# Kernel optimization log

Hardware: AMD Instinct MI355X
Metric: run time of the kernel (lower is better)

Reference implementation:

```python
import jax, jax.numpy as jnp
import numpy as np

N_EMBD = 1024
N_HEAD = 16
B, T = 4, 2048

def setup_inputs() -> dict:
    key = jax.random.key(0)
    ks = jax.random.split(key, 5)
    s_attn = 1.0 / np.sqrt(N_EMBD)
    s_proj = 1.0 / np.sqrt(N_EMBD)
    return {
        "x": jax.random.normal(ks[0], (B, T, N_EMBD), dtype=jnp.float32),
        "w_attn": jax.random.uniform(ks[1], (N_EMBD, 3 * N_EMBD), jnp.float32, -s_attn, s_attn),
        "b_attn": jax.random.uniform(ks[2], (3 * N_EMBD,), jnp.float32, -s_attn, s_attn),
        "w_proj": jax.random.uniform(ks[3], (N_EMBD, N_EMBD), jnp.float32, -s_proj, s_proj),
        "b_proj": jax.random.uniform(ks[4], (N_EMBD,), jnp.float32, -s_proj, s_proj),
    }

def reference(x, w_attn, b_attn, w_proj, b_proj):
    Bx, Tx, C = x.shape
    hd = C // N_HEAD  # head dim
    qkv = x @ w_attn + b_attn                       # [B,T,3C]
    q, k, v = jnp.split(qkv, 3, axis=-1)
    # [B,T,C] -> [B,H,T,hd]
    def heads(t):
        return t.reshape(Bx, Tx, N_HEAD, hd).transpose(0, 2, 1, 3)
    q, k, v = heads(q), heads(k), heads(v)
    att = jnp.einsum('bhqd,bhkd->bhqk', q, k) * (1.0 / np.sqrt(hd))
    causal = jnp.tril(jnp.ones((Tx, Tx), dtype=bool))
    att = jnp.where(causal, att, -jnp.inf)
    att = jax.nn.softmax(att, axis=-1)
    y = jnp.einsum('bhqk,bhkd->bhqd', att, v)       # [B,H,T,hd]
    y = y.transpose(0, 2, 1, 3).reshape(Bx, Tx, C)
    return y @ w_proj + b_proj
```

## Files before the change

### kernel.cpp

```cpp
#include <hip/hip_runtime.h>
#include <cstdint>

typedef unsigned short u16;
typedef short s16x8 __attribute__((ext_vector_type(8)));
typedef short s16x4 __attribute__((ext_vector_type(4)));
typedef float f32x4 __attribute__((ext_vector_type(4)));
typedef float f32x16 __attribute__((ext_vector_type(16)));

#define B_   4
#define T_   2048
#define C_   1024
#define H_   16
#define HD_  64
#define M_   8192
#define N3_  3072

#define QSCALE 0.18033688011112042f

__device__ inline u16 f2b(float f) {
  union { float f; uint32_t u; } v; v.f = f;
  uint32_t u = v.u;
  return (u16)((u + 0x7FFFu + ((u >> 16) & 1u)) >> 16);
}

__device__ inline uint32_t cvtpk(float lo, float hi) {
  uint32_t r;
  asm("v_cvt_pk_bf16_f32 %0, %1, %2" : "=v"(r) : "v"(lo), "v"(hi));
  return r;
}

__device__ inline void gload_lds16(const void* g, void* l) {
  __builtin_amdgcn_global_load_lds(
      (const __attribute__((address_space(1))) void*)g,
      (__attribute__((address_space(3))) void*)l, 16, 0, 0);
}

__global__ __launch_bounds__(256) void cvt_f32_bf16(
    const float* __restrict__ in, u16* __restrict__ out, int n) {
  int i = (blockIdx.x * 256 + threadIdx.x) * 8;
  if (i >= n) return;
  float4 a = *(const float4*)(in + i);
  float4 b = *(const float4*)(in + i + 4);
  s16x8 r;
  r[0] = (short)f2b(a.x); r[1] = (short)f2b(a.y);
  r[2] = (short)f2b(a.z); r[3] = (short)f2b(a.w);
  r[4] = (short)f2b(b.x); r[5] = (short)f2b(b.y);
  r[6] = (short)f2b(b.z); r[7] = (short)f2b(b.w);
  *(s16x8*)(out + i) = r;
}

__global__ __launch_bounds__(256) void cvt_transpose(
    const float* __restrict__ W, u16* __restrict__ WT, int K, int N) {
  __shared__ u16 tile[64][65];
  int n0 = blockIdx.x * 64, k0 = blockIdx.y * 64;
  int j = threadIdx.x & 63, i0 = threadIdx.x >> 6;
#pragma unroll
  for (int i = i0; i < 64; i += 4)
    tile[i][j] = f2b(W[(size_t)(k0 + i) * N + n0 + j]);
  __syncthreads();
#pragma unroll
  for (int i = i0; i < 64; i += 4)
    WT[(size_t)(n0 + i) * K + k0 + j] = tile[j][i];
}

template <int MODE>
__global__ __launch_bounds__(256, 4) void gemm_bt(
    const u16* __restrict__ A, const u16* __restrict__ Bt,
    const float* __restrict__ bias, float* __restrict__ outf,
    u16* __restrict__ qo, u16* __restrict__ ko, u16* __restrict__ vo,
    int M, int N, int K) {
  __shared__ u16 As[128 * 64];
  __shared__ u16 Bs[128 * 64];

  int nwg = gridDim.x;
  int bid0 = blockIdx.x;
  int bid = (bid0 & 7) * (nwg >> 3) + (bid0 >> 3);
  int nbn = N >> 7;
  int bm = bid / nbn, bn = bid % nbn;
  int m0 = bm * 128, n0 = bn * 128;
  int tid = threadIdx.x;
  int lane = tid & 63, w = tid >> 6;
  int wm = (w >> 1) * 64, wn = (w & 1) * 64;
  int l15 = lane & 15, g = lane >> 4;

  f32x4 acc[4][4] = {};

  for (int kb = 0; kb < K; kb += 64) {
    __syncthreads();
#pragma unroll
    for (int p = 0; p < 4; ++p) {
      int idx = p * 256 + tid;
      int row = idx >> 3, pc = idx & 7;
      int sc = (pc ^ (row & 7)) * 8;
      gload_lds16(A  + (size_t)(m0 + row) * K + kb + sc, &As[idx * 8]);
      gload_lds16(Bt + (size_t)(n0 + row) * K + kb + sc, &Bs[idx * 8]);
    }
    __syncthreads();

#pragma unroll
    for (int ks = 0; ks < 2; ++ks) {
      int ck = ((g + 4 * ks) ^ (l15 & 7)) * 8;
      s16x8 af[4], bf[4];
#pragma unroll
      for (int mi = 0; mi < 4; ++mi)
        af[mi] = *(const s16x8*)&As[(wm + mi * 16 + l15) * 64 + ck];
#pragma unroll
      for (int ni = 0; ni < 4; ++ni)
        bf[ni] = *(const s16x8*)&Bs[(wn + ni * 16 + l15) * 64 + ck];
#pragma unroll
      for (int mi = 0; mi < 4; ++mi)
#pragma unroll
        for (int ni = 0; ni < 4; ++ni)
          acc[mi][ni] = __builtin_amdgcn_mfma_f32_16x16x32_bf16(
              af[mi], bf[ni], acc[mi][ni], 0, 0, 0);
    }
  }

#pragma unroll
  for (int mi = 0; mi < 4; ++mi)
#pragma unroll
    for (int ni = 0; ni < 4; ++ni) {
      int col = n0 + wn + ni * 16 + l15;
      float bv = bias[col];
      int row0 = m0 + wm + mi * 16 + g * 4;
      if (MODE == 0) {
#pragma unroll
        for (int r = 0; r < 4; ++r)
          outf[(size_t)(row0 + r) * N + col] = acc[mi][ni][r] + bv;
      } else {
        int which = col >> 10, hc = col & 1023;
        int h = hc >> 6, d = hc & 63;
        int b = row0 >> 11, t0 = row0 & 2047;
        if (which == 2) {
          s16x4 pv;
#pragma unroll
          for (int r = 0; r < 4; ++r) pv[r] = (short)f2b(acc[mi][ni][r] + bv);
          *(s16x4*)(vo + ((size_t)((b * 16 + h) * 64 + d)) * 2048 + t0) = pv;
        } else {
          u16* dst = (which == 0) ? qo : ko;
          float sc2 = (which == 0) ? QSCALE : 1.0f;
#pragma unroll
          for (int r = 0; r < 4; ++r)
            dst[(((size_t)(b * 16 + h)) * 2048 + (t0 + r)) * 64 + d] =
                f2b((acc[mi][ni][r] + bv) * sc2);
        }
      }
    }
}

__global__ __launch_bounds__(256, 3) void attn_fwd(
    const u16* __restrict__ Q, const u16* __restrict__ Kg,
    const u16* __restrict__ Vt, u16* __restrict__ Y) {
  __shared__ u16 Ks[64 * 64];
  __shared__ u16 Vs[64 * 64];

  int bid = blockIdx.x;
  int bh = bid & 63;
  int qb = 15 - (bid >> 6);
  int tid = threadIdx.x, lane = tid & 63, w = tid >> 6;
  int l31 = lane & 31, half = lane >> 5;

  const u16* Qh = Q  + (size_t)bh * T_ * HD_;
  const u16* Kh = Kg + (size_t)bh * T_ * HD_;
  const u16* Vh = Vt + (size_t)bh * HD_ * T_;

  int q0 = qb * 128;
  int qw = q0 + w * 32;
  int qrow = qw + l31;

  s16x8 qa[4];
#pragma unroll
  for (int kst = 0; kst < 4; ++kst)
    qa[kst] = *(const s16x8*)(Qh + (size_t)qrow * HD_ + kst * 16 + half * 8);

  f32x16 oacc[2] = {};
  float m = -3.0e30f, l = 0.f;

  int sr = tid >> 3, sc = tid & 7;
  int wswz = (sr & 7) << 4;
  int rswz = (l31 & 7) << 4;
  char* KsB = (char*)Ks;
  char* VsB = (char*)Vs;

  s16x8 kr0 = *(const s16x8*)(Kh + (size_t)sr * HD_ + sc * 8);
  s16x8 kr1 = *(const s16x8*)(Kh + (size_t)(sr + 32) * HD_ + sc * 8);
  s16x8 vr0 = *(const s16x8*)(Vh + (size_t)sr * T_ + sc * 8);
  s16x8 vr1 = *(const s16x8*)(Vh + (size_t)(sr + 32) * T_ + sc * 8);

  int ntile = 2 * qb + 2;
  for (int kt = 0; kt < ntile; ++kt) {
    int kvb = kt * 64;
    __syncthreads();
    *(s16x8*)(KsB + sr * 128 + ((sc * 16) ^ wswz))        = kr0;
    *(s16x8*)(KsB + (sr + 32) * 128 + ((sc * 16) ^ wswz)) = kr1;
    *(s16x8*)(VsB + sr * 128 + ((sc * 16) ^ wswz))        = vr0;
    *(s16x8*)(VsB + (sr + 32) * 128 + ((sc * 16) ^ wswz)) = vr1;
    __syncthreads();

    {
      int kvn = (kt + 1 < ntile) ? (kt + 1) * 64 : 0;
      kr0 = *(const s16x8*)(Kh + (size_t)(kvn + sr) * HD_ + sc * 8);
      kr1 = *(const s16x8*)(Kh + (size_t)(kvn + sr + 32) * HD_ + sc * 8);
      vr0 = *(const s16x8*)(Vh + (size_t)sr * T_ + kvn + sc * 8);
      vr1 = *(const s16x8*)(Vh + (size_t)(sr + 32) * T_ + kvn + sc * 8);
    }

    if (kvb > qw + 31) continue;

    f32x16 s0 = {}, s1 = {};
    __builtin_amdgcn_s_setprio(1);
#pragma unroll
    for (int kst = 0; kst < 4; ++kst) {
      s16x8 kb0 = *(const s16x8*)(KsB +
          (((l31) * 128 + kst * 32 + half * 16) ^ rswz));
      s0 = __builtin_amdgcn_mfma_f32_32x32x16_bf16(kb0, qa[kst], s0, 0, 0, 0);
      s16x8 kb1 = *(const s16x8*)(KsB +
          (((32 + l31) * 128 + kst * 32 + half * 16) ^ rswz));
      s1 = __builtin_amdgcn_mfma_f32_32x32x16_bf16(kb1, qa[kst], s1, 0, 0, 0);
    }
    __builtin_amdgcn_s_setprio(0);

    if (kvb + 63 > qw) {
#pragma unroll
      for (int r = 0; r < 16; ++r) {
        int kv0 = kvb + (r & 3) + 8 * (r >> 2) + 4 * half;
        if (kv0 > qrow) s0[r] = -1e30f;
        if (kv0 + 32 > qrow) s1[r] = -1e30f;
      }
    }

    float a0 = fmaxf(fmaxf(s0[0], s0[1]), fmaxf(s0[2], s0[3]));
    float a1 = fmaxf(fmaxf(s0[4], s0[5]), fmaxf(s0[6], s0[7]));
    float a2 = fmaxf(fmaxf(s0[8], s0[9]), fmaxf(s0[10], s0[11]));
    float a3 = fmaxf(fmaxf(s0[12], s0[13]), fmaxf(s0[14], s0[15]));
    float a4 = fmaxf(fmaxf(s1[0], s1[1]), fmaxf(s1[2], s1[3]));
    float a5 = fmaxf(fmaxf(s1[4], s1[5]), fmaxf(s1[6], s1[7]));
    float a6 = fmaxf(fmaxf(s1[8], s1[9]), fmaxf(s1[10], s1[11]));
    float a7 = fmaxf(fmaxf(s1[12], s1[13]), fmaxf(s1[14], s1[15]));
    float mx = fmaxf(fmaxf(fmaxf(a0, a1), fmaxf(a2, a3)),
                     fmaxf(fmaxf(a4, a5), fmaxf(a6, a7)));
    mx = fmaxf(mx, __shfl_xor(mx, 32, 64));

    if (!__all(mx <= m + 8.0f)) {
      float mn = fmaxf(m, mx);
      float alpha = __builtin_amdgcn_exp2f(m - mn);
      m = mn;
      l *= alpha;
#pragma unroll
      for (int i = 0; i < 16; ++i) { oacc[0][i] *= alpha; oacc[1][i] *= alpha; }
    }

    float rs = 0.f;
#pragma unroll
    for (int r = 0; r < 16; ++r) {
      float p0 = __builtin_amdgcn_exp2f(s0[r] - m);
      float p1 = __builtin_amdgcn_exp2f(s1[r] - m);
      s0[r] = p0; s1[r] = p1;
      rs += p0 + p1;
    }
    rs += __shfl_xor(rs, 32, 64);
    l += rs;

    s16x8 pb[4];
#pragma unroll
    for (int ks4 = 0; ks4 < 4; ++ks4) {
      const f32x16& sv = (ks4 < 2) ? s0 : s1;
      const int R = (ks4 & 1) * 8;
      uint32_t A0 = cvtpk(sv[R + 0], sv[R + 1]);
      uint32_t A1 = cvtpk(sv[R + 2], sv[R + 3]);
      uint32_t B0 = cvtpk(sv[R + 4], sv[R + 5]);
      uint32_t B1 = cvtpk(sv[R + 6], sv[R + 7]);
      uint32_t r0 = (uint32_t)__shfl_xor((int)(half ? A0 : B0), 32, 64);
      uint32_t r1 = (uint32_t)__shfl_xor((int)(half ? A1 : B1), 32, 64);
      union { uint32_t u[4]; s16x8 v; } pk_;
      pk_.u[0] = half ? r0 : A0;
      pk_.u[1] = half ? r1 : A1;
      pk_.u[2] = half ? B0 : r0;
      pk_.u[3] = half ? B1 : r1;
      pb[ks4] = pk_.v;
    }

    __builtin_amdgcn_s_setprio(1);
#pragma unroll
    for (int hb = 0; hb < 2; ++hb)
#pragma unroll
      for (int ks4 = 0; ks4 < 4; ++ks4) {
        s16x8 va = *(const s16x8*)(VsB +
            (((hb * 32 + l31) * 128 + ks4 * 32 + half * 16) ^ rswz));
        oacc[hb] = __builtin_amdgcn_mfma_f32_32x32x16_bf16(va, pb[ks4],
                                                           oacc[hb], 0, 0, 0);
      }
    __builtin_amdgcn_s_setprio(0);
  }

  int b = bh >> 4, h = bh & 15;
  float inv = 1.0f / l;
  u16* yrow = Y + ((size_t)b * T_ + qrow) * C_ + h * 64;
#pragma unroll
  for (int hb = 0; hb < 2; ++hb)
#pragma unroll
    for (int rg = 0; rg < 4; ++rg) {
      union { uint32_t u[2]; s16x4 v; } o;
      o.u[0] = cvtpk(oacc[hb][rg * 4 + 0] * inv, oacc[hb][rg * 4 + 1] * inv);
      o.u[1] = cvtpk(oacc[hb][rg * 4 + 2] * inv, oacc[hb][rg * 4 + 3] * inv);
      *(s16x4*)(yrow + hb * 32 + rg * 8 + half * 4) = o.v;
    }
}

extern "C" void kernel_launch(void* const* d_in, const int* in_sizes, int n_in,
                              void* d_out, int out_size, void* d_ws, size_t ws_size,
                              hipStream_t stream) {
  const float* x      = (const float*)d_in[0];
  const float* w_attn = (const float*)d_in[1];
  const float* b_attn = (const float*)d_in[2];
  const float* w_proj = (const float*)d_in[3];
  const float* b_proj = (const float*)d_in[4];
  float* out = (float*)d_out;

  u16* ws  = (u16*)d_ws;
  u16* xb  = ws;
  u16* wat = xb  + (size_t)M_ * C_;
  u16* wpt = wat + (size_t)N3_ * C_;
  u16* q   = wpt + (size_t)C_ * C_;
  u16* k   = q   + (size_t)M_ * C_;
  u16* v   = k   + (size_t)M_ * C_;
  u16* ya  = xb;

  cvt_f32_bf16<<<dim3((M_ * C_) / (256 * 8)), dim3(256), 0, stream>>>(x, xb, M_ * C_);
  cvt_transpose<<<dim3(N3_ / 64, C_ / 64), dim3(256), 0, stream>>>(w_attn, wat, C_, N3_);
  cvt_transpose<<<dim3(C_ / 64, C_ / 64), dim3(256), 0, stream>>>(w_proj, wpt, C_, C_);

  gemm_bt<1><<<dim3((M_ / 128) * (N3_ / 128)), dim3(256), 0, stream>>>(
      xb, wat, b_attn, nullptr, q, k, v, M_, N3_, C_);

  attn_fwd<<<dim3(64 * 16), dim3(256), 0, stream>>>(q, k, v, ya);

  gemm_bt<0><<<dim3((M_ / 128) * (C_ / 128)), dim3(256), 0, stream>>>(
      ya, wpt, b_proj, out, nullptr, nullptr, nullptr, M_, C_, C_);
}
```

Measured before the change: 166.5 us.

## Double-buffer attention K/V tiles in LDS with direct global-to-LDS loads

```diff
diff --git a/kernel.cpp b/kernel.cpp
--- a/kernel.cpp
+++ b/kernel.cpp
@@ -151,8 +151,8 @@
 __global__ __launch_bounds__(256, 3) void attn_fwd(
     const u16* __restrict__ Q, const u16* __restrict__ Kg,
     const u16* __restrict__ Vt, u16* __restrict__ Y) {
-  __shared__ u16 Ks[64 * 64];
-  __shared__ u16 Vs[64 * 64];
+  __shared__ u16 Ks[2][64 * 64];
+  __shared__ u16 Vs[2][64 * 64];
 
   int bid = blockIdx.x;
   int bh = bid & 63;
@@ -176,122 +176,120 @@
   f32x16 oacc[2] = {};
   float m = -3.0e30f, l = 0.f;
 
-  int sr = tid >> 3, sc = tid & 7;
-  int wswz = (sr & 7) << 4;
+  int srow = tid >> 3;
+  int sc = ((tid & 7) ^ (srow & 7)) * 8;
   int rswz = (l31 & 7) << 4;
-  char* KsB = (char*)Ks;
-  char* VsB = (char*)Vs;
-
-  s16x8 kr0 = *(const s16x8*)(Kh + (size_t)sr * HD_ + sc * 8);
-  s16x8 kr1 = *(const s16x8*)(Kh + (size_t)(sr + 32) * HD_ + sc * 8);
-  s16x8 vr0 = *(const s16x8*)(Vh + (size_t)sr * T_ + sc * 8);
-  s16x8 vr1 = *(const s16x8*)(Vh + (size_t)(sr + 32) * T_ + sc * 8);
+
+#define STAGE(bb, kvb_) do { \
+  gload_lds16(Kh + (size_t)((kvb_) + srow) * HD_ + sc,      &Ks[bb][tid * 8]); \
+  gload_lds16(Kh + (size_t)((kvb_) + 32 + srow) * HD_ + sc, &Ks[bb][(256 + tid) * 8]); \
+  gload_lds16(Vh + (size_t)srow * T_ + (kvb_) + sc,         &Vs[bb][tid * 8]); \
+  gload_lds16(Vh + (size_t)(32 + srow) * T_ + (kvb_) + sc,  &Vs[bb][(256 + tid) * 8]); \
+} while (0)
 
   int ntile = 2 * qb + 2;
+  STAGE(0, 0);
+  __syncthreads();
+
   for (int kt = 0; kt < ntile; ++kt) {
+    int cur = kt & 1;
     int kvb = kt * 64;
+    int kvn = (kt + 1 < ntile) ? (kt + 1) * 64 : 0;
+    STAGE(cur ^ 1, kvn);
+
+    if (kvb <= qw + 31) {
+      char* KsB = (char*)Ks[cur];
+      char* VsB = (char*)Vs[cur];
+
+      f32x16 s0 = {}, s1 = {};
+      __builtin_amdgcn_s_setprio(1);
+#pragma unroll
+      for (int kst = 0; kst < 4; ++kst) {
+        s16x8 kb0 = *(const s16x8*)(KsB +
+            ((l31 * 128 + kst * 32 + half * 16) ^ rswz));
+        s0 = __builtin_amdgcn_mfma_f32_32x32x16_bf16(kb0, qa[kst], s0, 0, 0, 0);
+        s16x8 kb1 = *(const s16x8*)(KsB +
+            (((32 + l31) * 128 + kst * 32 + half * 16) ^ rswz));
+        s1 = __builtin_amdgcn_mfma_f32_32x32x16_bf16(kb1, qa[kst], s1, 0, 0, 0);
+      }
+      __builtin_amdgcn_s_setprio(0);
+
+      if (kvb + 63 > qw) {
+#pragma unroll
+        for (int r = 0; r < 16; ++r) {
+          int kv0 = kvb + (r & 3) + 8 * (r >> 2) + 4 * half;
+          if (kv0 > qrow) s0[r] = -1e30f;
+          if (kv0 + 32 > qrow) s1[r] = -1e30f;
+        }
+      }
+
+      float a0 = fmaxf(fmaxf(s0[0], s0[1]), fmaxf(s0[2], s0[3]));
+      float a1 = fmaxf(fmaxf(s0[4], s0[5]), fmaxf(s0[6], s0[7]));
+      float a2 = fmaxf(fmaxf(s0[8], s0[9]), fmaxf(s0[10], s0[11]));
+      float a3 = fmaxf(fmaxf(s0[12], s0[13]), fmaxf(s0[14], s0[15]));
+      float a4 = fmaxf(fmaxf(s1[0], s1[1]), fmaxf(s1[2], s1[3]));
+      float a5 = fmaxf(fmaxf(s1[4], s1[5]), fmaxf(s1[6], s1[7]));
+      float a6 = fmaxf(fmaxf(s1[8], s1[9]), fmaxf(s1[10], s1[11]));
+      float a7 = fmaxf(fmaxf(s1[12], s1[13]), fmaxf(s1[14], s1[15]));
+      float mx = fmaxf(fmaxf(fmaxf(a0, a1), fmaxf(a2, a3)),
+                       fmaxf(fmaxf(a4, a5), fmaxf(a6, a7)));
+      mx = fmaxf(mx, __shfl_xor(mx, 32, 64));
+
+      if (!__all(mx <= m + 8.0f)) {
+        float mn = fmaxf(m, mx);
+        float alpha = __builtin_amdgcn_exp2f(m - mn);
+        m = mn;
+        l *= alpha;
+#pragma unroll
+        for (int i = 0; i < 16; ++i) { oacc[0][i] *= alpha; oacc[1][i] *= alpha; }
+      }
+
+      float rs = 0.f;
+#pragma unroll
+      for (int r = 0; r < 16; ++r) {
+        float p0 = __builtin_amdgcn_exp2f(s0[r] - m);
+        float p1 = __builtin_amdgcn_exp2f(s1[r] - m);
+        s0[r] = p0; s1[r] = p1;
+        rs += p0 + p1;
+      }
+      rs += __shfl_xor(rs, 32, 64);
+      l += rs;
+
+      s16x8 pb[4];
+#pragma unroll
+      for (int ks4 = 0; ks4 < 4; ++ks4) {
+        const f32x16& sv = (ks4 < 2) ? s0 : s1;
+        const int R = (ks4 & 1) * 8;
+        uint32_t A0 = cvtpk(sv[R + 0], sv[R + 1]);
+        uint32_t A1 = cvtpk(sv[R + 2], sv[R + 3]);
+        uint32_t B0 = cvtpk(sv[R + 4], sv[R + 5]);
+        uint32_t B1 = cvtpk(sv[R + 6], sv[R + 7]);
+        uint32_t r0 = (uint32_t)__shfl_xor((int)(half ? A0 : B0), 32, 64);
+        uint32_t r1 = (uint32_t)__shfl_xor((int)(half ? A1 : B1), 32, 64);
+        union { uint32_t u[4]; s16x8 v; } pk_;
+        pk_.u[0] = half ? r0 : A0;
+        pk_.u[1] = half ? r1 : A1;
+        pk_.u[2] = half ? B0 : r0;
+        pk_.u[3] = half ? B1 : r1;
+        pb[ks4] = pk_.v;
+      }
+
+      __builtin_amdgcn_s_setprio(1);
+#pragma unroll
+      for (int hb = 0; hb < 2; ++hb)
+#pragma unroll
+        for (int ks4 = 0; ks4 < 4; ++ks4) {
+          s16x8 va = *(const s16x8*)(VsB +
+              (((hb * 32 + l31) * 128 + ks4 * 32 + half * 16) ^ rswz));
+          oacc[hb] = __builtin_amdgcn_mfma_f32_32x32x16_bf16(va, pb[ks4],
+                                                             oacc[hb], 0, 0, 0);
+        }
+      __builtin_amdgcn_s_setprio(0);
+    }
+
     __syncthreads();
-    *(s16x8*)(KsB + sr * 128 + ((sc * 16) ^ wswz))        = kr0;
-    *(s16x8*)(KsB + (sr + 32) * 128 + ((sc * 16) ^ wswz)) = kr1;
-    *(s16x8*)(VsB + sr * 128 + ((sc * 16) ^ wswz))        = vr0;
-    *(s16x8*)(VsB + (sr + 32) * 128 + ((sc * 16) ^ wswz)) = vr1;
-    __syncthreads();
-
-    {
-      int kvn = (kt + 1 < ntile) ? (kt + 1) * 64 : 0;
-      kr0 = *(const s16x8*)(Kh + (size_t)(kvn + sr) * HD_ + sc * 8);
-      kr1 = *(const s16x8*)(Kh + (size_t)(kvn + sr + 32) * HD_ + sc * 8);
-      vr0 = *(const s16x8*)(Vh + (size_t)sr * T_ + kvn + sc * 8);
-      vr1 = *(const s16x8*)(Vh + (size_t)(sr + 32) * T_ + kvn + sc * 8);
-    }
-
-    if (kvb > qw + 31) continue;
-
-    f32x16 s0 = {}, s1 = {};
-    __builtin_amdgcn_s_setprio(1);
-#pragma unroll
-    for (int kst = 0; kst < 4; ++kst) {
-      s16x8 kb0 = *(const s16x8*)(KsB +
-          (((l31) * 128 + kst * 32 + half * 16) ^ rswz));
-      s0 = __builtin_amdgcn_mfma_f32_32x32x16_bf16(kb0, qa[kst], s0, 0, 0, 0);
-      s16x8 kb1 = *(const s16x8*)(KsB +
-          (((32 + l31) * 128 + kst * 32 + half * 16) ^ rswz));
-      s1 = __builtin_amdgcn_mfma_f32_32x32x16_bf16(kb1, qa[kst], s1, 0, 0, 0);
-    }
-    __builtin_amdgcn_s_setprio(0);
-
-    if (kvb + 63 > qw) {
-#pragma unroll
-      for (int r = 0; r < 16; ++r) {
-        int kv0 = kvb + (r & 3) + 8 * (r >> 2) + 4 * half;
-        if (kv0 > qrow) s0[r] = -1e30f;
-        if (kv0 + 32 > qrow) s1[r] = -1e30f;
-      }
-    }
-
-    float a0 = fmaxf(fmaxf(s0[0], s0[1]), fmaxf(s0[2], s0[3]));
-    float a1 = fmaxf(fmaxf(s0[4], s0[5]), fmaxf(s0[6], s0[7]));
-    float a2 = fmaxf(fmaxf(s0[8], s0[9]), fmaxf(s0[10], s0[11]));
-    float a3 = fmaxf(fmaxf(s0[12], s0[13]), fmaxf(s0[14], s0[15]));
-    float a4 = fmaxf(fmaxf(s1[0], s1[1]), fmaxf(s1[2], s1[3]));
-    float a5 = fmaxf(fmaxf(s1[4], s1[5]), fmaxf(s1[6], s1[7]));
-    float a6 = fmaxf(fmaxf(s1[8], s1[9]), fmaxf(s1[10], s1[11]));
-    float a7 = fmaxf(fmaxf(s1[12], s1[13]), fmaxf(s1[14], s1[15]));
-    float mx = fmaxf(fmaxf(fmaxf(a0, a1), fmaxf(a2, a3)),
-                     fmaxf(fmaxf(a4, a5), fmaxf(a6, a7)));
-    mx = fmaxf(mx, __shfl_xor(mx, 32, 64));
-
-    if (!__all(mx <= m + 8.0f)) {
-      float mn = fmaxf(m, mx);
-      float alpha = __builtin_amdgcn_exp2f(m - mn);
-      m = mn;
-      l *= alpha;
-#pragma unroll
-      for (int i = 0; i < 16; ++i) { oacc[0][i] *= alpha; oacc[1][i] *= alpha; }
-    }
-
-    float rs = 0.f;
-#pragma unroll
-    for (int r = 0; r < 16; ++r) {
-      float p0 = __builtin_amdgcn_exp2f(s0[r] - m);
-      float p1 = __builtin_amdgcn_exp2f(s1[r] - m);
-      s0[r] = p0; s1[r] = p1;
-      rs += p0 + p1;
-    }
-    rs += __shfl_xor(rs, 32, 64);
-    l += rs;
-
-    s16x8 pb[4];
-#pragma unroll
-    for (int ks4 = 0; ks4 < 4; ++ks4) {
-      const f32x16& sv = (ks4 < 2) ? s0 : s1;
-      const int R = (ks4 & 1) * 8;
-      uint32_t A0 = cvtpk(sv[R + 0], sv[R + 1]);
-      uint32_t A1 = cvtpk(sv[R + 2], sv[R + 3]);
-      uint32_t B0 = cvtpk(sv[R + 4], sv[R + 5]);
-      uint32_t B1 = cvtpk(sv[R + 6], sv[R + 7]);
-      uint32_t r0 = (uint32_t)__shfl_xor((int)(half ? A0 : B0), 32, 64);
-      uint32_t r1 = (uint32_t)__shfl_xor((int)(half ? A1 : B1), 32, 64);
-      union { uint32_t u[4]; s16x8 v; } pk_;
-      pk_.u[0] = half ? r0 : A0;
-      pk_.u[1] = half ? r1 : A1;
-      pk_.u[2] = half ? B0 : r0;
-      pk_.u[3] = half ? B1 : r1;
-      pb[ks4] = pk_.v;
-    }
-
-    __builtin_amdgcn_s_setprio(1);
-#pragma unroll
-    for (int hb = 0; hb < 2; ++hb)
-#pragma unroll
-      for (int ks4 = 0; ks4 < 4; ++ks4) {
-        s16x8 va = *(const s16x8*)(VsB +
-            (((hb * 32 + l31) * 128 + ks4 * 32 + half * 16) ^ rswz));
-        oacc[hb] = __builtin_amdgcn_mfma_f32_32x32x16_bf16(va, pb[ks4],
-                                                           oacc[hb], 0, 0, 0);
-      }
-    __builtin_amdgcn_s_setprio(0);
   }
+#undef STAGE
 
   int b = bh >> 4, h = bh & 15;
   float inv = 1.0f / l;
```

Result: slower. 174.2 us (+4.6%).
